# Kernel tuning notes

Hardware: AMD Instinct MI355X
Metric: run time of the kernel (lower is better)

Reference implementation:

```python
import jax, jax.numpy as jnp
import numpy as np

B, P, LANE_LEN = 16, 512, 20
C, T, H, DEPTH = 128, 64, 192, 3
NTL, NLT = 9, 20


def _mlp(x, w1, b1, w2, b2):
    h = jax.nn.gelu(x @ w1 + b1, approximate=False)  # torch nn.GELU = exact erf
    return h @ w2 + b2


def _ln(x, w, b, eps=1e-5):
    m = x.mean(-1, keepdims=True)
    v = jnp.var(x, axis=-1, keepdims=True)
    return (x - m) * jax.lax.rsqrt(v + eps) * w + b


def setup_inputs() -> dict:
    key = jax.random.key(0)
    ks = iter(jax.random.split(key, 40))

    def p(*shape):
        return 0.02 * jax.random.normal(next(ks), shape, dtype=jnp.float32)

    return {
        'x': jax.random.normal(next(ks), (B, P, LANE_LEN, 5), dtype=jnp.float32),
        'tl_table': p(NTL, C),
        'lane_table': p(NLT, C),
        'ch_fc1_w': p(4, C), 'ch_fc1_b': jnp.zeros(C),
        'ch_fc2_w': p(C, C), 'ch_fc2_b': jnp.zeros(C),
        'tok_fc1_w': p(LANE_LEN, T), 'tok_fc1_b': jnp.zeros(T),
        'tok_fc2_w': p(T, T), 'tok_fc2_b': jnp.zeros(T),
        'blk_norm1_w': jnp.ones((DEPTH, C)), 'blk_norm1_b': jnp.zeros((DEPTH, C)),
        'blk_tok_fc1_w': p(DEPTH, T, T), 'blk_tok_fc1_b': jnp.zeros((DEPTH, T)),
        'blk_tok_fc2_w': p(DEPTH, T, T), 'blk_tok_fc2_b': jnp.zeros((DEPTH, T)),
        'blk_norm2_w': jnp.ones((DEPTH, C)), 'blk_norm2_b': jnp.zeros((DEPTH, C)),
        'blk_ch_fc1_w': p(DEPTH, C, C), 'blk_ch_fc1_b': jnp.zeros((DEPTH, C)),
        'blk_ch_fc2_w': p(DEPTH, C, C), 'blk_ch_fc2_b': jnp.zeros((DEPTH, C)),
        'norm_w': jnp.ones(C), 'norm_b': jnp.zeros(C),
        'emb_fc1_w': p(C, H), 'emb_fc1_b': jnp.zeros(H),
        'emb_fc2_w': p(H, H), 'emb_fc2_b': jnp.zeros(H),
    }


def reference(x, tl_table, lane_table, ch_fc1_w, ch_fc1_b, ch_fc2_w, ch_fc2_b,
              tok_fc1_w, tok_fc1_b, tok_fc2_w, tok_fc2_b,
              blk_norm1_w, blk_norm1_b, blk_tok_fc1_w, blk_tok_fc1_b,
              blk_tok_fc2_w, blk_tok_fc2_b, blk_norm2_w, blk_norm2_b,
              blk_ch_fc1_w, blk_ch_fc1_b, blk_ch_fc2_w, blk_ch_fc2_b,
              norm_w, norm_b, emb_fc1_w, emb_fc1_b, emb_fc2_w, emb_fc2_b):
    b, p_, v, _ = x.shape
    mid = x[:, :, LANE_LEN // 2, :]  # [B,P,5]
    pos = jnp.stack([mid[..., 0], mid[..., 1], mid[..., 2],
                     mid[..., 3] / (NTL - 1), mid[..., 4] / (NLT - 1)], axis=-1)
    hdg = x[..., 2]
    geom = jnp.concatenate([x[..., 0:2], jnp.cos(hdg)[..., None], jnp.sin(hdg)[..., None]], axis=-1)  # [B,P,V,4]
    mask_v = jnp.sum(geom != 0, axis=-1) == 0
    mask_p = jnp.all(mask_v, axis=-1)  # [B,P] True = fully padded polyline
    valid = (~mask_p).reshape(-1)
    # jit-friendly equivalent of gather->compute->scatter: compute all rows, zero invalid ones
    g = geom.reshape(b * p_, v, 4)
    tl = jnp.clip(x[..., 3].reshape(b * p_, v).astype(jnp.int32), 0, NTL - 1)
    lt = jnp.clip(x[..., 4].reshape(b * p_, v).astype(jnp.int32), 0, NLT - 1)
    f = _mlp(g, ch_fc1_w, ch_fc1_b, ch_fc2_w, ch_fc2_b) + tl_table[tl] + lane_table[lt]  # [N,V,C]
    f = _mlp(f.transpose(0, 2, 1), tok_fc1_w, tok_fc1_b, tok_fc2_w, tok_fc2_b).transpose(0, 2, 1)  # [N,T,C]
    for i in range(DEPTH):
        y = _ln(f, blk_norm1_w[i], blk_norm1_b[i])
        y = _mlp(y.transpose(0, 2, 1), blk_tok_fc1_w[i], blk_tok_fc1_b[i],
                 blk_tok_fc2_w[i], blk_tok_fc2_b[i]).transpose(0, 2, 1)
        f = f + y
        y = _ln(f, blk_norm2_w[i], blk_norm2_b[i])
        f = f + _mlp(y, blk_ch_fc1_w[i], blk_ch_fc1_b[i], blk_ch_fc2_w[i], blk_ch_fc2_b[i])
    f = f.mean(axis=1)  # [N,C]
    f = _mlp(_ln(f, norm_w, norm_b), emb_fc1_w, emb_fc1_b, emb_fc2_w, emb_fc2_b)  # [N,H]
    out = (f * valid[:, None].astype(f.dtype)).reshape(b, p_, H)
    return out, mask_p, pos
```

## Files before the change

kernel.cpp:

```cpp
#include <hip/hip_runtime.h>

#define NROWS 8192
#define V 20
#define C 128
#define T 64
#define HDIM 192
#define DEPTH 3

typedef __attribute__((ext_vector_type(8))) short bf16x8;
typedef __attribute__((ext_vector_type(4))) float floatx4;

#define WS_TOKFC1 0
#define WS_TOKFC2 2048
#define WS_BTOK1  6144
#define WS_BTOK2  18432
#define WS_CHFC2  30720
#define WS_BCH1   47104
#define WS_BCH2   96256
#define WS_TOTAL  145408

__device__ __forceinline__ float bf2f(unsigned short u) {
    union { unsigned int i; float f; } c; c.i = ((unsigned int)u) << 16; return c.f;
}
__device__ __forceinline__ unsigned short f2bf(float f) {
    union { float f; unsigned int i; } c; c.f = f;
    unsigned int r = c.i + 0x7fffu + ((c.i >> 16) & 1u);
    return (unsigned short)(r >> 16);
}
__device__ __forceinline__ float gelu(float x) {
    float u = x * x;
    float p = fmaf(u, 0.044715f, 1.0f);
    float arg = x * p * -2.3022042f;
    float e = __builtin_amdgcn_exp2f(arg);
    return x * __builtin_amdgcn_rcpf(1.0f + e);
}
__device__ __forceinline__ floatx4 mfma16(bf16x8 a, bf16x8 b, floatx4 c) {
    return __builtin_amdgcn_mfma_f32_16x16x32_bf16(a, b, c, 0, 0, 0);
}


__device__ __forceinline__ void ln_reg(const floatx4 (&R)[8],
                                       const float* __restrict__ w,
                                       const float* __restrict__ b,
                                       unsigned short* __restrict__ s1,
                                       int wid, int lrow, int rrow, bool transposed)
{
    float s[4], q[4];
#pragma unroll
    for (int rr = 0; rr < 4; ++rr) {
        float ss = 0.f, qq = 0.f;
#pragma unroll
        for (int nt = 0; nt < 8; ++nt) { float v = R[nt][rr]; ss += v; qq += v * v; }
        s[rr] = ss; q[rr] = qq;
    }
#pragma unroll
    for (int rr = 0; rr < 4; ++rr) {
        s[rr] += __shfl_xor(s[rr], 1);  q[rr] += __shfl_xor(q[rr], 1);
        s[rr] += __shfl_xor(s[rr], 2);  q[rr] += __shfl_xor(q[rr], 2);
        s[rr] += __shfl_xor(s[rr], 4);  q[rr] += __shfl_xor(q[rr], 4);
        s[rr] += __shfl_xor(s[rr], 8);  q[rr] += __shfl_xor(q[rr], 8);
    }
    float m[4], rs[4];
#pragma unroll
    for (int rr = 0; rr < 4; ++rr) {
        m[rr] = s[rr] * (1.f / 128.f);
        rs[rr] = rsqrtf(q[rr] * (1.f / 128.f) - m[rr] * m[rr] + 1e-5f);
    }
#pragma unroll
    for (int nt = 0; nt < 8; ++nt) {
        const int c = 16 * nt + lrow;
        const float wv = w[c], bv = b[c];
#pragma unroll
        for (int rr = 0; rr < 4; ++rr) {
            const int t = 16 * wid + rrow + rr;
            unsigned short o = f2bf((R[nt][rr] - m[rr]) * rs[rr] * wv + bv);
            if (transposed) s1[c * 72 + t] = o;
            else            s1[t * 136 + c] = o;
        }
    }
}

__device__ __forceinline__ void tok_fc1_gelu(unsigned short* __restrict__ s1,
                                             const unsigned short* __restrict__ wB,
                                             const float* __restrict__ bias,
                                             int wid, int lrow, int kq, int rrow)
{
#pragma unroll
    for (int mt = 0; mt < 2; ++mt) {
        bf16x8 at[2];
#pragma unroll
        for (int kc = 0; kc < 2; ++kc)
            at[kc] = *(const bf16x8*)(s1 + (32 * wid + mt * 16 + lrow) * 72 + kc * 32 + kq);
        floatx4 acc[4];
#pragma unroll
        for (int nt = 0; nt < 4; ++nt) acc[nt] = {0.f, 0.f, 0.f, 0.f};
#pragma unroll
        for (int nt = 0; nt < 4; ++nt)
#pragma unroll
            for (int kc = 0; kc < 2; ++kc) {
                bf16x8 b = *(const bf16x8*)(wB + (nt * 16 + lrow) * 64 + kc * 32 + kq);
                acc[nt] = mfma16(at[kc], b, acc[nt]);
            }
#pragma unroll
        for (int nt = 0; nt < 4; ++nt) {
            const int t = nt * 16 + lrow;
            const float bb = bias[t];
#pragma unroll
            for (int rr = 0; rr < 4; ++rr)
                s1[(32 * wid + mt * 16 + rrow + rr) * 72 + t] = f2bf(gelu(acc[nt][rr] + bb));
        }
    }
}

__device__ __forceinline__ void tok_fc2_to_R(const unsigned short* __restrict__ s1,
                                             const unsigned short* __restrict__ wB,
                                             const float* __restrict__ bias,
                                             floatx4 (&R)[8],
                                             int wid, int lrow, int kq, int rrow)
{
    bf16x8 aw[2];
#pragma unroll
    for (int kc = 0; kc < 2; ++kc)
        aw[kc] = *(const bf16x8*)(wB + (16 * wid + lrow) * 64 + kc * 32 + kq);
    float bb[4];
#pragma unroll
    for (int rr = 0; rr < 4; ++rr) bb[rr] = bias[16 * wid + rrow + rr];
#pragma unroll
    for (int nt = 0; nt < 8; ++nt) {
        floatx4 acc = R[nt];
#pragma unroll
        for (int kc = 0; kc < 2; ++kc) {
            bf16x8 b = *(const bf16x8*)(s1 + (16 * nt + lrow) * 72 + kc * 32 + kq);
            acc = mfma16(aw[kc], b, acc);
        }
#pragma unroll
        for (int rr = 0; rr < 4; ++rr) acc[rr] += bb[rr];
        R[nt] = acc;
    }
}

__device__ __forceinline__ void ch_fc1_gelu(unsigned short* __restrict__ s1,
                                            const unsigned short* __restrict__ wB,
                                            const float* __restrict__ bias,
                                            int wid, int lrow, int kq, int rrow)
{
    bf16x8 a2[4];
    const int m = 16 * wid + lrow;
#pragma unroll
    for (int kc = 0; kc < 4; ++kc)
        a2[kc] = *(const bf16x8*)(s1 + m * 136 + kc * 32 + kq);
#pragma unroll
    for (int g = 0; g < 4; ++g) {
        floatx4 acc[2];
#pragma unroll
        for (int i = 0; i < 2; ++i) acc[i] = {0.f, 0.f, 0.f, 0.f};
#pragma unroll
        for (int i = 0; i < 2; ++i) {
            const int n = (2 * g + i) * 16 + lrow;
#pragma unroll
            for (int kc = 0; kc < 4; ++kc) {
                bf16x8 b = *(const bf16x8*)(wB + n * 128 + kc * 32 + kq);
                acc[i] = mfma16(a2[kc], b, acc[i]);
            }
        }
#pragma unroll
        for (int i = 0; i < 2; ++i) {
            const int c = (2 * g + i) * 16 + lrow;
            const float bb = bias[c];
#pragma unroll
            for (int rr = 0; rr < 4; ++rr)
                s1[(16 * wid + rrow + rr) * 136 + c] = f2bf(gelu(acc[i][rr] + bb));
        }
    }
}

__device__ __forceinline__ void ch_fc2_to_R(const unsigned short* __restrict__ s1,
                                            const unsigned short* __restrict__ wB,
                                            const float* __restrict__ bias,
                                            floatx4 (&R)[8],
                                            int wid, int lrow, int kq, int rrow)
{
    bf16x8 a2[4];
    const int m = 16 * wid + lrow;
#pragma unroll
    for (int kc = 0; kc < 4; ++kc)
        a2[kc] = *(const bf16x8*)(s1 + m * 136 + kc * 32 + kq);
#pragma unroll
    for (int nt = 0; nt < 8; ++nt) {
        floatx4 acc = R[nt];
        const float bb = bias[16 * nt + lrow];
#pragma unroll
        for (int kc = 0; kc < 4; ++kc) {
            bf16x8 b = *(const bf16x8*)(wB + (16 * nt + lrow) * 128 + kc * 32 + kq);
            acc = mfma16(a2[kc], b, acc);
        }
#pragma unroll
        for (int rr = 0; rr < 4; ++rr) acc[rr] += bb;
        R[nt] = acc;
    }
}

__device__ __forceinline__ void layer_norm_to(const float* __restrict__ sF,
                                              unsigned short* __restrict__ sA,
                                              const float* __restrict__ w,
                                              const float* __restrict__ b,
                                              int tid, bool transposed, int strideOut)
{
    const int t = tid >> 2, part = tid & 3;
    const float* row = sF + t * 132 + part * 32;
    float s = 0.f, q = 0.f;
#pragma unroll
    for (int j = 0; j < 8; ++j) {
        float4 v = *(const float4*)(row + j * 4);
        s += (v.x + v.y) + (v.z + v.w);
        q += v.x * v.x + v.y * v.y + v.z * v.z + v.w * v.w;
    }
    s += __shfl_xor(s, 1); q += __shfl_xor(q, 1);
    s += __shfl_xor(s, 2); q += __shfl_xor(q, 2);
    const float m = s * (1.f / 128.f);
    const float rs = rsqrtf(q * (1.f / 128.f) - m * m + 1e-5f);
#pragma unroll
    for (int j = 0; j < 8; ++j) {
        float4 v = *(const float4*)(row + j * 4);
        const int c = part * 32 + j * 4;
        float4 wv = *(const float4*)(w + c);
        float4 bv = *(const float4*)(b + c);
        unsigned short o0 = f2bf((v.x - m) * rs * wv.x + bv.x);
        unsigned short o1 = f2bf((v.y - m) * rs * wv.y + bv.y);
        unsigned short o2 = f2bf((v.z - m) * rs * wv.z + bv.z);
        unsigned short o3 = f2bf((v.w - m) * rs * wv.w + bv.w);
        if (transposed) {
            sA[(c + 0) * strideOut + t] = o0;
            sA[(c + 1) * strideOut + t] = o1;
            sA[(c + 2) * strideOut + t] = o2;
            sA[(c + 3) * strideOut + t] = o3;
        } else {
            ushort4 pk; pk.x = o0; pk.y = o1; pk.z = o2; pk.w = o3;
            *(ushort4*)(sA + t * strideOut + c) = pk;
        }
    }
}

__global__ void prep_weights(const float* __restrict__ tokfc1,
                             const float* __restrict__ tokfc2,
                             const float* __restrict__ btok1,
                             const float* __restrict__ btok2,
                             const float* __restrict__ chfc2,
                             const float* __restrict__ bch1,
                             const float* __restrict__ bch2,
                             unsigned short* __restrict__ ws)
{
    int idx = blockIdx.x * 256 + threadIdx.x;
    if (idx >= WS_TOTAL) return;
    if (idx < 2048) {
        int n = idx >> 5, k = idx & 31;
        ws[WS_TOKFC1 + idx] = (k < V) ? f2bf(tokfc1[k * 64 + n]) : 0;
        return;
    }
    idx -= 2048;
    if (idx < 4096) {
        int n = idx >> 6, k = idx & 63;
        ws[WS_TOKFC2 + idx] = f2bf(tokfc2[k * 64 + n]);
        return;
    }
    idx -= 4096;
    if (idx < 12288) {
        int d = idx >> 12, rem = idx & 4095, n = rem >> 6, k = rem & 63;
        ws[WS_BTOK1 + idx] = f2bf(btok1[d * 4096 + k * 64 + n]);
        return;
    }
    idx -= 12288;
    if (idx < 12288) {
        int d = idx >> 12, rem = idx & 4095, n = rem >> 6, k = rem & 63;
        ws[WS_BTOK2 + idx] = f2bf(btok2[d * 4096 + k * 64 + n]);
        return;
    }
    idx -= 12288;
    if (idx < 16384) {
        int n = idx >> 7, k = idx & 127;
        ws[WS_CHFC2 + idx] = f2bf(chfc2[k * 128 + n]);
        return;
    }
    idx -= 16384;
    if (idx < 49152) {
        int d = idx >> 14, rem = idx & 16383, n = rem >> 7, k = rem & 127;
        ws[WS_BCH1 + idx] = f2bf(bch1[d * 16384 + k * 128 + n]);
        return;
    }
    idx -= 49152;
    {
        int d = idx >> 14, rem = idx & 16383, n = rem >> 7, k = rem & 127;
        ws[WS_BCH2 + idx] = f2bf(bch2[d * 16384 + k * 128 + n]);
    }
}

__global__ __launch_bounds__(256) __attribute__((amdgpu_waves_per_eu(3)))
void lanefusion_mfma(
    const float* __restrict__ x,
    const float* __restrict__ tl_table, const float* __restrict__ lane_table,
    const float* __restrict__ ch_fc1_w, const float* __restrict__ ch_fc1_b,
    const float* __restrict__ ch_fc2_b,
    const float* __restrict__ tok_fc1_b, const float* __restrict__ tok_fc2_b,
    const float* __restrict__ bn1w, const float* __restrict__ bn1b,
    const float* __restrict__ btok1b, const float* __restrict__ btok2b,
    const float* __restrict__ bn2w, const float* __restrict__ bn2b,
    const float* __restrict__ bch1b, const float* __restrict__ bch2b,
    const float* __restrict__ norm_w, const float* __restrict__ norm_b,
    const float* __restrict__ emb1w, const float* __restrict__ emb1b,
    const float* __restrict__ emb2w, const float* __restrict__ emb2b,
    const unsigned short* __restrict__ ws,
    float* __restrict__ out)
{
    __shared__ unsigned short s1[128 * 72];
    __shared__ float sVec[320];
    __shared__ int sTL[V], sLT[V], sMaskV[V];
    __shared__ float sValidF;

    const int tid = threadIdx.x;
    const int r = blockIdx.x;
    const int lane = tid & 63, wid = tid >> 6;
    const int lrow = lane & 15;
    const int kq = (lane >> 4) * 8;
    const int rrow = (lane >> 4) * 4;

    float* outp  = out;
    float* maskp = out + (size_t)NROWS * HDIM;
    float* posp  = maskp + NROWS;

    float* sX = sVec;
    float* sG = sVec + 128;

    {
        uint4* p = (uint4*)s1;
        uint4 z; z.x = z.y = z.z = z.w = 0u;
        for (int i = tid; i < 1152; i += 256) p[i] = z;
    }

    const float* xr = x + (size_t)r * (V * 5);
    if (tid < V * 5) sX[tid] = xr[tid];
    __syncthreads();

    if (tid < V) {
        float x0 = sX[tid * 5 + 0], x1 = sX[tid * 5 + 1], hd = sX[tid * 5 + 2];
        float chv = cosf(hd), shv = sinf(hd);
        sG[tid * 4 + 0] = x0; sG[tid * 4 + 1] = x1;
        sG[tid * 4 + 2] = chv; sG[tid * 4 + 3] = shv;
        int nz = (x0 != 0.f) + (x1 != 0.f) + (chv != 0.f) + (shv != 0.f);
        sMaskV[tid] = (nz == 0);
        int tl = (int)sX[tid * 5 + 3]; tl = tl < 0 ? 0 : (tl > 8 ? 8 : tl);
        int lt = (int)sX[tid * 5 + 4]; lt = lt < 0 ? 0 : (lt > 19 ? 19 : lt);
        sTL[tid] = tl; sLT[tid] = lt;
    }
    __syncthreads();

    if (tid == 0) {
        int mp = 1;
        for (int v = 0; v < V; ++v) mp &= sMaskV[v];
        sValidF = mp ? 0.f : 1.f;
        maskp[r] = mp ? 1.f : 0.f;
        posp[(size_t)r * 5 + 0] = sX[50];
        posp[(size_t)r * 5 + 1] = sX[51];
        posp[(size_t)r * 5 + 2] = sX[52];
        posp[(size_t)r * 5 + 3] = sX[53] * (1.f / 8.f);
        posp[(size_t)r * 5 + 4] = sX[54] * (1.f / 19.f);
    }

    {
        float g0[4], g1[4];
        const bool v1ok = (lrow < 4);
        const int v0 = lrow, v1 = 16 + lrow;
#pragma unroll
        for (int i = 0; i < 4; ++i) {
            g0[i] = sG[v0 * 4 + i];
            g1[i] = v1ok ? sG[v1 * 4 + i] : 0.f;
        }
        floatx4 acc[2][2];
#pragma unroll
        for (int mt = 0; mt < 2; ++mt)
#pragma unroll
            for (int ni = 0; ni < 2; ++ni) acc[mt][ni] = {0.f, 0.f, 0.f, 0.f};
        const unsigned short* wB = ws + WS_CHFC2;
#pragma unroll 1
        for (int kc = 0; kc < 4; ++kc) {
            union { unsigned short u[8]; bf16x8 v; } p0, p1;
            const int kb = kc * 32 + kq;
#pragma unroll
            for (int j = 0; j < 8; ++j) {
                const float w0 = ch_fc1_w[0 * C + kb + j];
                const float w1 = ch_fc1_w[1 * C + kb + j];
                const float w2 = ch_fc1_w[2 * C + kb + j];
                const float w3 = ch_fc1_w[3 * C + kb + j];
                const float bb = ch_fc1_b[kb + j];
                float h0 = fmaf(g0[0], w0, fmaf(g0[1], w1, fmaf(g0[2], w2, fmaf(g0[3], w3, bb))));
                p0.u[j] = f2bf(gelu(h0));
                if (v1ok) {
                    float h1 = fmaf(g1[0], w0, fmaf(g1[1], w1, fmaf(g1[2], w2, fmaf(g1[3], w3, bb))));
                    p1.u[j] = f2bf(gelu(h1));
                } else p1.u[j] = 0;
            }
#pragma unroll
            for (int ni = 0; ni < 2; ++ni) {
                const int n = (2 * wid + ni) * 16 + lrow;
                bf16x8 b = *(const bf16x8*)(wB + n * 128 + kc * 32 + kq);
                acc[0][ni] = mfma16(p0.v, b, acc[0][ni]);
                acc[1][ni] = mfma16(p1.v, b, acc[1][ni]);
            }
        }
#pragma unroll
        for (int ni = 0; ni < 2; ++ni) {
            const int c = (2 * wid + ni) * 16 + lrow;
            const float bb = ch_fc2_b[c];
#pragma unroll
            for (int mt = 0; mt < 2; ++mt)
#pragma unroll
                for (int rr = 0; rr < 4; ++rr) {
                    const int v = mt * 16 + rrow + rr;
                    if (v < V) {
                        float val = acc[mt][ni][rr] + bb
                                  + tl_table[sTL[v] * C + c] + lane_table[sLT[v] * C + c];
                        s1[c * 72 + v] = f2bf(val);
                    }
                }
        }
    }

    {
        bf16x8 af[2];
#pragma unroll
        for (int mt = 0; mt < 2; ++mt) {
            const int m = 32 * wid + mt * 16 + lrow;
            af[mt] = *(const bf16x8*)(s1 + m * 72 + kq);
        }
        floatx4 acc[2][4];
#pragma unroll
        for (int mt = 0; mt < 2; ++mt)
#pragma unroll
            for (int nt = 0; nt < 4; ++nt) acc[mt][nt] = {0.f, 0.f, 0.f, 0.f};
        const unsigned short* wB = ws + WS_TOKFC1;
#pragma unroll
        for (int nt = 0; nt < 4; ++nt) {
            const int n = nt * 16 + lrow;
            bf16x8 b = *(const bf16x8*)(wB + n * 32 + kq);
            acc[0][nt] = mfma16(af[0], b, acc[0][nt]);
            acc[1][nt] = mfma16(af[1], b, acc[1][nt]);
        }
#pragma unroll
        for (int nt = 0; nt < 4; ++nt) {
            const int t = nt * 16 + lrow;
            const float bb = tok_fc1_b[t];
#pragma unroll
            for (int mt = 0; mt < 2; ++mt)
#pragma unroll
                for (int rr = 0; rr < 4; ++rr) {
                    const int m = 32 * wid + mt * 16 + rrow + rr;
                    s1[m * 72 + t] = f2bf(gelu(acc[mt][nt][rr] + bb));
                }
        }
    }
    __syncthreads();

    floatx4 R[8];
#pragma unroll
    for (int nt = 0; nt < 8; ++nt) R[nt] = {0.f, 0.f, 0.f, 0.f};

    tok_fc2_to_R(s1, ws + WS_TOKFC2, tok_fc2_b, R, wid, lrow, kq, rrow);

#pragma unroll 1
    for (int blk = 0; blk < DEPTH; ++blk) {
        __syncthreads();
        ln_reg(R, bn1w + blk * C, bn1b + blk * C, s1, wid, lrow, rrow, true);
        __syncthreads();
        tok_fc1_gelu(s1, ws + WS_BTOK1 + blk * 4096, btok1b + blk * T, wid, lrow, kq, rrow);
        __syncthreads();
        tok_fc2_to_R(s1, ws + WS_BTOK2 + blk * 4096, btok2b + blk * T, R, wid, lrow, kq, rrow);
        __syncthreads();
        ln_reg(R, bn2w + blk * C, bn2b + blk * C, s1, wid, lrow, rrow, false);
        ch_fc1_gelu(s1, ws + WS_BCH1 + blk * 16384, bch1b + blk * C, wid, lrow, kq, rrow);
        ch_fc2_to_R(s1, ws + WS_BCH2 + blk * 16384, bch2b + blk * C, R, wid, lrow, kq, rrow);
    }
    __syncthreads();

    {
        float* P = (float*)s1;
        float snt[8];
#pragma unroll
        for (int nt = 0; nt < 8; ++nt)
            snt[nt] = (R[nt][0] + R[nt][1]) + (R[nt][2] + R[nt][3]);
#pragma unroll
        for (int nt = 0; nt < 8; ++nt) {
            snt[nt] += __shfl_xor(snt[nt], 16);
            snt[nt] += __shfl_xor(snt[nt], 32);
        }
        if (lane < 16) {
#pragma unroll
            for (int nt = 0; nt < 8; ++nt)
                P[wid * 128 + 16 * nt + lane] = snt[nt];
        }
    }
    __syncthreads();
    float fm = 0.f;
    {
        const float* P = (const float*)s1;
        if (tid < C) {
            fm = (P[tid] + P[128 + tid] + P[256 + tid] + P[384 + tid]) * (1.f / 64.f);
            sVec[tid] = fm;
        }
    }
    __syncthreads();
    {
        float s = 0.f, q = 0.f;
#pragma unroll
        for (int c = 0; c < C; c += 4) {
            float4 v = *(const float4*)(sVec + c);
            s += (v.x + v.y) + (v.z + v.w);
            q += v.x * v.x + v.y * v.y + v.z * v.z + v.w * v.w;
        }
        __syncthreads();
        const float m = s * (1.f / 128.f);
        const float rs = rsqrtf(q * (1.f / 128.f) - m * m + 1e-5f);
        if (tid < C) sVec[tid] = (fm - m) * rs * norm_w[tid] + norm_b[tid];
    }
    __syncthreads();

    if (tid < HDIM) {
        float a0 = 0.f, a1 = 0.f, a2 = 0.f, a3 = 0.f;
#pragma unroll 4
        for (int c = 0; c < C; c += 4) {
            float4 sv = *(const float4*)(sVec + c);
            a0 = fmaf(sv.x, emb1w[(c + 0) * HDIM + tid], a0);
            a1 = fmaf(sv.y, emb1w[(c + 1) * HDIM + tid], a1);
            a2 = fmaf(sv.z, emb1w[(c + 2) * HDIM + tid], a2);
            a3 = fmaf(sv.w, emb1w[(c + 3) * HDIM + tid], a3);
        }
        sVec[C + tid] = gelu(((a0 + a1) + (a2 + a3)) + emb1b[tid]);
    }
    __syncthreads();
    if (tid < HDIM) {
        float a0 = 0.f, a1 = 0.f, a2 = 0.f, a3 = 0.f;
#pragma unroll 4
        for (int j = 0; j < HDIM; j += 4) {
            float4 sv = *(const float4*)(sVec + C + j);
            a0 = fmaf(sv.x, emb2w[(j + 0) * HDIM + tid], a0);
            a1 = fmaf(sv.y, emb2w[(j + 1) * HDIM + tid], a1);
            a2 = fmaf(sv.z, emb2w[(j + 2) * HDIM + tid], a2);
            a3 = fmaf(sv.w, emb2w[(j + 3) * HDIM + tid], a3);
        }
        outp[(size_t)r * HDIM + tid] = (((a0 + a1) + (a2 + a3)) + emb2b[tid]) * sValidF;
    }
}

template<int K, int LDA, int N>
__device__ __forceinline__ void gemm_bf(const unsigned short* __restrict__ A,
                                        const float* __restrict__ W,
                                        float acc[4][8])
{
#pragma unroll 2
    for (int k = 0; k < K; k += 4) {
        float a[4][4];
#pragma unroll
        for (int i = 0; i < 4; ++i) {
            ushort4 raw = *(const ushort4*)(A + i * LDA + k);
            a[i][0] = bf2f(raw.x); a[i][1] = bf2f(raw.y);
            a[i][2] = bf2f(raw.z); a[i][3] = bf2f(raw.w);
        }
#pragma unroll
        for (int kk = 0; kk < 4; ++kk) {
            const float* wr = W + (k + kk) * N;
            float4 w0 = *(const float4*)(wr);
            float4 w1 = *(const float4*)(wr + 4);
#pragma unroll
            for (int i = 0; i < 4; ++i) {
                acc[i][0] = fmaf(a[i][kk], w0.x, acc[i][0]);
                acc[i][1] = fmaf(a[i][kk], w0.y, acc[i][1]);
                acc[i][2] = fmaf(a[i][kk], w0.z, acc[i][2]);
                acc[i][3] = fmaf(a[i][kk], w0.w, acc[i][3]);
                acc[i][4] = fmaf(a[i][kk], w1.x, acc[i][4]);
                acc[i][5] = fmaf(a[i][kk], w1.y, acc[i][5]);
                acc[i][6] = fmaf(a[i][kk], w1.z, acc[i][6]);
                acc[i][7] = fmaf(a[i][kk], w1.w, acc[i][7]);
            }
        }
    }
}

template<int K, int LDA, int N>
__device__ __forceinline__ void gemm_f32(const float* __restrict__ A,
                                         const float* __restrict__ W,
                                         float acc[4][8])
{
#pragma unroll
    for (int k = 0; k < K; k += 4) {
        float a[4][4];
#pragma unroll
        for (int i = 0; i < 4; ++i) {
            float4 v = *(const float4*)(A + i * LDA + k);
            a[i][0] = v.x; a[i][1] = v.y; a[i][2] = v.z; a[i][3] = v.w;
        }
#pragma unroll
        for (int kk = 0; kk < 4; ++kk) {
            const float* wr = W + (k + kk) * N;
            float4 w0 = *(const float4*)(wr);
            float4 w1 = *(const float4*)(wr + 4);
#pragma unroll
            for (int i = 0; i < 4; ++i) {
                acc[i][0] = fmaf(a[i][kk], w0.x, acc[i][0]);
                acc[i][1] = fmaf(a[i][kk], w0.y, acc[i][1]);
                acc[i][2] = fmaf(a[i][kk], w0.z, acc[i][2]);
                acc[i][3] = fmaf(a[i][kk], w0.w, acc[i][3]);
                acc[i][4] = fmaf(a[i][kk], w1.x, acc[i][4]);
                acc[i][5] = fmaf(a[i][kk], w1.y, acc[i][5]);
                acc[i][6] = fmaf(a[i][kk], w1.z, acc[i][6]);
                acc[i][7] = fmaf(a[i][kk], w1.w, acc[i][7]);
            }
        }
    }
}

__global__ __launch_bounds__(256, 3)
void lanefusion_scalar(
    const float* __restrict__ x,
    const float* __restrict__ tl_table, const float* __restrict__ lane_table,
    const float* __restrict__ ch_fc1_w, const float* __restrict__ ch_fc1_b,
    const float* __restrict__ ch_fc2_w, const float* __restrict__ ch_fc2_b,
    const float* __restrict__ tok_fc1_w, const float* __restrict__ tok_fc1_b,
    const float* __restrict__ tok_fc2_w, const float* __restrict__ tok_fc2_b,
    const float* __restrict__ bn1w, const float* __restrict__ bn1b,
    const float* __restrict__ btok1w, const float* __restrict__ btok1b,
    const float* __restrict__ btok2w, const float* __restrict__ btok2b,
    const float* __restrict__ bn2w, const float* __restrict__ bn2b,
    const float* __restrict__ bch1w, const float* __restrict__ bch1b,
// ... 153 lines not shown
#pragma unroll
                for (int j = 0; j < 8; ++j)
                    sF[(c0 + j) * 132 + (r0 + i)] += acc[i][j] + btok2b[blk * T + c0 + j];
        }
        __syncthreads();

        layer_norm_to(sF, sA, bn2w + blk * C, bn2b + blk * C, tid, false, 132);
        __syncthreads();
        {
            const int r0 = (tid >> 4) * 4, c0 = (tid & 15) * 8;
            float acc[4][8] = {};
            gemm_bf<128, 132, 128>(sA + r0 * 132, bch1w + blk * C * C + c0, acc);
#pragma unroll
            for (int i = 0; i < 4; ++i)
#pragma unroll
                for (int j = 0; j < 8; ++j)
                    acc[i][j] = gelu(acc[i][j] + bch1b[blk * C + c0 + j]);
            __syncthreads();
#pragma unroll
            for (int i = 0; i < 4; ++i)
#pragma unroll
                for (int j = 0; j < 8; ++j)
                    sA[(r0 + i) * 132 + c0 + j] = f2bf(acc[i][j]);
        }
        __syncthreads();
        {
            const int r0 = (tid >> 4) * 4, c0 = (tid & 15) * 8;
            float acc[4][8] = {};
            gemm_bf<128, 132, 128>(sA + r0 * 132, bch2w + blk * C * C + c0, acc);
#pragma unroll
            for (int i = 0; i < 4; ++i)
#pragma unroll
                for (int j = 0; j < 8; ++j)
                    sF[(r0 + i) * 132 + c0 + j] += acc[i][j] + bch2b[blk * C + c0 + j];
        }
        __syncthreads();
    }

    float fm = 0.f;
    if (tid < C) {
#pragma unroll 8
        for (int t = 0; t < T; ++t) fm += sF[t * 132 + tid];
        fm *= (1.f / 64.f);
        sVec[tid] = fm;
    }
    __syncthreads();
    {
        float s = 0.f, q = 0.f;
        for (int c = 0; c < C; ++c) { float v = sVec[c]; s += v; q += v * v; }
        __syncthreads();
        const float m = s * (1.f / 128.f);
        const float rs = rsqrtf(q * (1.f / 128.f) - m * m + 1e-5f);
        if (tid < C) sVec[tid] = (fm - m) * rs * norm_w[tid] + norm_b[tid];
    }
    __syncthreads();

    if (tid < HDIM) {
        float v1 = emb1b[tid];
        for (int c = 0; c < C; ++c) v1 = fmaf(sVec[c], emb1w[c * HDIM + tid], v1);
        sVec[C + tid] = gelu(v1);
    }
    __syncthreads();
    if (tid < HDIM) {
        float v2 = emb2b[tid];
        for (int j = 0; j < HDIM; ++j) v2 = fmaf(sVec[C + j], emb2w[j * HDIM + tid], v2);
        outp[(size_t)r * HDIM + tid] = v2 * sValidF;
    }
}

extern "C" void kernel_launch(void* const* d_in, const int* in_sizes, int n_in,
                              void* d_out, int out_size, void* d_ws, size_t ws_size,
                              hipStream_t stream) {
    (void)in_sizes; (void)n_in; (void)out_size;
    if (ws_size >= (size_t)WS_TOTAL * 2) {
        prep_weights<<<dim3((WS_TOTAL + 255) / 256), dim3(256), 0, stream>>>(
            (const float*)d_in[7],
            (const float*)d_in[9],
            (const float*)d_in[13],
            (const float*)d_in[15],
            (const float*)d_in[5],
            (const float*)d_in[19],
            (const float*)d_in[21],
            (unsigned short*)d_ws);
        lanefusion_mfma<<<dim3(NROWS), dim3(256), 0, stream>>>(
            (const float*)d_in[0],  (const float*)d_in[1],  (const float*)d_in[2],
            (const float*)d_in[3],  (const float*)d_in[4],
            (const float*)d_in[6],
            (const float*)d_in[8],  (const float*)d_in[10],
            (const float*)d_in[11], (const float*)d_in[12],
            (const float*)d_in[14], (const float*)d_in[16],
            (const float*)d_in[17], (const float*)d_in[18],
            (const float*)d_in[20], (const float*)d_in[22],
            (const float*)d_in[23], (const float*)d_in[24],
            (const float*)d_in[25], (const float*)d_in[26],
            (const float*)d_in[27], (const float*)d_in[28],
            (const unsigned short*)d_ws,
            (float*)d_out);
    } else {
        lanefusion_scalar<<<dim3(NROWS), dim3(256), 0, stream>>>(
            (const float*)d_in[0],  (const float*)d_in[1],  (const float*)d_in[2],
            (const float*)d_in[3],  (const float*)d_in[4],  (const float*)d_in[5],
            (const float*)d_in[6],  (const float*)d_in[7],  (const float*)d_in[8],
            (const float*)d_in[9],  (const float*)d_in[10], (const float*)d_in[11],
            (const float*)d_in[12], (const float*)d_in[13], (const float*)d_in[14],
            (const float*)d_in[15], (const float*)d_in[16], (const float*)d_in[17],
            (const float*)d_in[18], (const float*)d_in[19], (const float*)d_in[20],
            (const float*)d_in[21], (const float*)d_in[22], (const float*)d_in[23],
            (const float*)d_in[24], (const float*)d_in[25], (const float*)d_in[26],
            (const float*)d_in[27], (const float*)d_in[28],
            (float*)d_out);
    }
}
```

Before: 1.192 ms.

## Process two polylines per block with two waves per row and register-reused weight fragments

Each block now handles two rows, with waves split into pairs per row, so each wave computes a 32-row M tile (two MFMA m-tiles). Weight fragments are loaded once and reused across both m-tiles, which halves weight traffic from global/L2 per row, and the grid is halved. In exchange, register pressure rises (R doubles to 16 floatx4), shared memory doubles, and the final embedding MLP is serialized over the two rows.

```diff
diff --git a/kernel.cpp b/kernel.cpp
--- a/kernel.cpp
+++ b/kernel.cpp
@@ -39,164 +39,192 @@
 }
 
 
-__device__ __forceinline__ void ln_reg(const floatx4 (&R)[8],
-                                       const float* __restrict__ w,
-                                       const float* __restrict__ b,
-                                       unsigned short* __restrict__ s1,
-                                       int wid, int lrow, int rrow, bool transposed)
-{
-    float s[4], q[4];
-#pragma unroll
-    for (int rr = 0; rr < 4; ++rr) {
-        float ss = 0.f, qq = 0.f;
-#pragma unroll
-        for (int nt = 0; nt < 8; ++nt) { float v = R[nt][rr]; ss += v; qq += v * v; }
-        s[rr] = ss; q[rr] = qq;
-    }
-#pragma unroll
-    for (int rr = 0; rr < 4; ++rr) {
-        s[rr] += __shfl_xor(s[rr], 1);  q[rr] += __shfl_xor(q[rr], 1);
-        s[rr] += __shfl_xor(s[rr], 2);  q[rr] += __shfl_xor(q[rr], 2);
-        s[rr] += __shfl_xor(s[rr], 4);  q[rr] += __shfl_xor(q[rr], 4);
-        s[rr] += __shfl_xor(s[rr], 8);  q[rr] += __shfl_xor(q[rr], 8);
-    }
-    float m[4], rs[4];
-#pragma unroll
-    for (int rr = 0; rr < 4; ++rr) {
-        m[rr] = s[rr] * (1.f / 128.f);
-        rs[rr] = rsqrtf(q[rr] * (1.f / 128.f) - m[rr] * m[rr] + 1e-5f);
-    }
-#pragma unroll
-    for (int nt = 0; nt < 8; ++nt) {
-        const int c = 16 * nt + lrow;
-        const float wv = w[c], bv = b[c];
+__device__ __forceinline__ void ln_reg2(const floatx4 (&R)[2][8],
+                                        const float* __restrict__ w,
+                                        const float* __restrict__ b,
+                                        unsigned short* __restrict__ s1r,
+                                        int vw, int lrow, int rrow, bool transposed)
+{
+#pragma unroll
+    for (int mt = 0; mt < 2; ++mt) {
+        float s[4], q[4];
 #pragma unroll
         for (int rr = 0; rr < 4; ++rr) {
-            const int t = 16 * wid + rrow + rr;
-            unsigned short o = f2bf((R[nt][rr] - m[rr]) * rs[rr] * wv + bv);
-            if (transposed) s1[c * 72 + t] = o;
-            else            s1[t * 136 + c] = o;
-        }
-    }
-}
-
-__device__ __forceinline__ void tok_fc1_gelu(unsigned short* __restrict__ s1,
-                                             const unsigned short* __restrict__ wB,
-                                             const float* __restrict__ bias,
-                                             int wid, int lrow, int kq, int rrow)
-{
-#pragma unroll
-    for (int mt = 0; mt < 2; ++mt) {
-        bf16x8 at[2];
+            float ss = 0.f, qq = 0.f;
+#pragma unroll
+            for (int nt = 0; nt < 8; ++nt) { float v = R[mt][nt][rr]; ss += v; qq += v * v; }
+            s[rr] = ss; q[rr] = qq;
+        }
+#pragma unroll
+        for (int rr = 0; rr < 4; ++rr) {
+            s[rr] += __shfl_xor(s[rr], 1);  q[rr] += __shfl_xor(q[rr], 1);
+            s[rr] += __shfl_xor(s[rr], 2);  q[rr] += __shfl_xor(q[rr], 2);
+            s[rr] += __shfl_xor(s[rr], 4);  q[rr] += __shfl_xor(q[rr], 4);
+            s[rr] += __shfl_xor(s[rr], 8);  q[rr] += __shfl_xor(q[rr], 8);
+        }
+        float m[4], rs[4];
+#pragma unroll
+        for (int rr = 0; rr < 4; ++rr) {
+            m[rr] = s[rr] * (1.f / 128.f);
+            rs[rr] = rsqrtf(q[rr] * (1.f / 128.f) - m[rr] * m[rr] + 1e-5f);
+        }
+#pragma unroll
+        for (int nt = 0; nt < 8; ++nt) {
+            const int c = 16 * nt + lrow;
+            const float wv = w[c], bv = b[c];
+#pragma unroll
+            for (int rr = 0; rr < 4; ++rr) {
+                const int t = 32 * vw + 16 * mt + rrow + rr;
+                unsigned short o = f2bf((R[mt][nt][rr] - m[rr]) * rs[rr] * wv + bv);
+                if (transposed) s1r[c * 72 + t] = o;
+                else            s1r[t * 136 + c] = o;
+            }
+        }
+    }
+}
+
+__device__ __forceinline__ void tok_fc1_g2(unsigned short* __restrict__ s1r,
+                                           const unsigned short* __restrict__ wB,
+                                           const float* __restrict__ bias,
+                                           int vw, int lrow, int kq, int rrow)
+{
+    bf16x8 bw[4][2];
+#pragma unroll
+    for (int nt = 0; nt < 4; ++nt)
 #pragma unroll
         for (int kc = 0; kc < 2; ++kc)
-            at[kc] = *(const bf16x8*)(s1 + (32 * wid + mt * 16 + lrow) * 72 + kc * 32 + kq);
+            bw[nt][kc] = *(const bf16x8*)(wB + (nt * 16 + lrow) * 64 + kc * 32 + kq);
+#pragma unroll 1
+    for (int mt = 0; mt < 4; ++mt) {
+        const int m = 64 * vw + 16 * mt + lrow;
+        bf16x8 af0 = *(const bf16x8*)(s1r + m * 72 + kq);
+        bf16x8 af1 = *(const bf16x8*)(s1r + m * 72 + 32 + kq);
         floatx4 acc[4];
 #pragma unroll
         for (int nt = 0; nt < 4; ++nt) acc[nt] = {0.f, 0.f, 0.f, 0.f};
 #pragma unroll
-        for (int nt = 0; nt < 4; ++nt)
-#pragma unroll
-            for (int kc = 0; kc < 2; ++kc) {
-                bf16x8 b = *(const bf16x8*)(wB + (nt * 16 + lrow) * 64 + kc * 32 + kq);
-                acc[nt] = mfma16(at[kc], b, acc[nt]);
-            }
+        for (int nt = 0; nt < 4; ++nt) {
+            acc[nt] = mfma16(af0, bw[nt][0], acc[nt]);
+            acc[nt] = mfma16(af1, bw[nt][1], acc[nt]);
+        }
 #pragma unroll
         for (int nt = 0; nt < 4; ++nt) {
             const int t = nt * 16 + lrow;
             const float bb = bias[t];
 #pragma unroll
             for (int rr = 0; rr < 4; ++rr)
-                s1[(32 * wid + mt * 16 + rrow + rr) * 72 + t] = f2bf(gelu(acc[nt][rr] + bb));
-        }
-    }
-}
-
-__device__ __forceinline__ void tok_fc2_to_R(const unsigned short* __restrict__ s1,
-                                             const unsigned short* __restrict__ wB,
-                                             const float* __restrict__ bias,
-                                             floatx4 (&R)[8],
-                                             int wid, int lrow, int kq, int rrow)
-{
-    bf16x8 aw[2];
-#pragma unroll
-    for (int kc = 0; kc < 2; ++kc)
-        aw[kc] = *(const bf16x8*)(wB + (16 * wid + lrow) * 64 + kc * 32 + kq);
-    float bb[4];
-#pragma unroll
-    for (int rr = 0; rr < 4; ++rr) bb[rr] = bias[16 * wid + rrow + rr];
+                s1r[(64 * vw + 16 * mt + rrow + rr) * 72 + t] = f2bf(gelu(acc[nt][rr] + bb));
+        }
+    }
+}
+
+__device__ __forceinline__ void tok_fc2_R2(const unsigned short* __restrict__ s1r,
+                                           const unsigned short* __restrict__ wB,
+                                           const float* __restrict__ bias,
+                                           floatx4 (&R)[2][8],
+                                           int vw, int lrow, int kq, int rrow)
+{
+    bf16x8 aw[2][2];
+#pragma unroll
+    for (int mt = 0; mt < 2; ++mt)
+#pragma unroll
+        for (int kc = 0; kc < 2; ++kc)
+            aw[mt][kc] = *(const bf16x8*)(wB + (32 * vw + 16 * mt + lrow) * 64 + kc * 32 + kq);
+    float bb[2][4];
+#pragma unroll
+    for (int mt = 0; mt < 2; ++mt)
+#pragma unroll
+        for (int rr = 0; rr < 4; ++rr) bb[mt][rr] = bias[32 * vw + 16 * mt + rrow + rr];
 #pragma unroll
     for (int nt = 0; nt < 8; ++nt) {
-        floatx4 acc = R[nt];
-#pragma unroll
-        for (int kc = 0; kc < 2; ++kc) {
-            bf16x8 b = *(const bf16x8*)(s1 + (16 * nt + lrow) * 72 + kc * 32 + kq);
-            acc = mfma16(aw[kc], b, acc);
-        }
-#pragma unroll
-        for (int rr = 0; rr < 4; ++rr) acc[rr] += bb[rr];
-        R[nt] = acc;
-    }
-}
-
-__device__ __forceinline__ void ch_fc1_gelu(unsigned short* __restrict__ s1,
-                                            const unsigned short* __restrict__ wB,
-                                            const float* __restrict__ bias,
-                                            int wid, int lrow, int kq, int rrow)
-{
-    bf16x8 a2[4];
-    const int m = 16 * wid + lrow;
-#pragma unroll
-    for (int kc = 0; kc < 4; ++kc)
-        a2[kc] = *(const bf16x8*)(s1 + m * 136 + kc * 32 + kq);
-#pragma unroll
+        bf16x8 b0 = *(const bf16x8*)(s1r + (16 * nt + lrow) * 72 + kq);
+        bf16x8 b1 = *(const bf16x8*)(s1r + (16 * nt + lrow) * 72 + 32 + kq);
+#pragma unroll
+        for (int mt = 0; mt < 2; ++mt) {
+            floatx4 acc = R[mt][nt];
+            acc = mfma16(aw[mt][0], b0, acc);
+            acc = mfma16(aw[mt][1], b1, acc);
+#pragma unroll
+            for (int rr = 0; rr < 4; ++rr) acc[rr] += bb[mt][rr];
+            R[mt][nt] = acc;
+        }
+    }
+}
+
+__device__ __forceinline__ void ch_fc1_g2(unsigned short* __restrict__ s1r,
+                                          const unsigned short* __restrict__ wB,
+                                          const float* __restrict__ bias,
+                                          int vw, int lrow, int kq, int rrow)
+{
+    bf16x8 a2[2][4];
+#pragma unroll
+    for (int mt = 0; mt < 2; ++mt) {
+        const int m = 32 * vw + 16 * mt + lrow;
+#pragma unroll
+        for (int kc = 0; kc < 4; ++kc)
+            a2[mt][kc] = *(const bf16x8*)(s1r + m * 136 + kc * 32 + kq);
+    }
+#pragma unroll 1
     for (int g = 0; g < 4; ++g) {
-        floatx4 acc[2];
-#pragma unroll
-        for (int i = 0; i < 2; ++i) acc[i] = {0.f, 0.f, 0.f, 0.f};
-#pragma unroll
-        for (int i = 0; i < 2; ++i) {
-            const int n = (2 * g + i) * 16 + lrow;
-#pragma unroll
-            for (int kc = 0; kc < 4; ++kc) {
-                bf16x8 b = *(const bf16x8*)(wB + n * 128 + kc * 32 + kq);
-                acc[i] = mfma16(a2[kc], b, acc[i]);
-            }
-        }
-#pragma unroll
-        for (int i = 0; i < 2; ++i) {
-            const int c = (2 * g + i) * 16 + lrow;
-            const float bb = bias[c];
-#pragma unroll
-            for (int rr = 0; rr < 4; ++rr)
-                s1[(16 * wid + rrow + rr) * 136 + c] = f2bf(gelu(acc[i][rr] + bb));
-        }
-    }
-}
-
-__device__ __forceinline__ void ch_fc2_to_R(const unsigned short* __restrict__ s1,
-                                            const unsigned short* __restrict__ wB,
-                                            const float* __restrict__ bias,
-                                            floatx4 (&R)[8],
-                                            int wid, int lrow, int kq, int rrow)
-{
-    bf16x8 a2[4];
-    const int m = 16 * wid + lrow;
-#pragma unroll
-    for (int kc = 0; kc < 4; ++kc)
-        a2[kc] = *(const bf16x8*)(s1 + m * 136 + kc * 32 + kq);
-#pragma unroll
+        bf16x8 bw[2][4];
+#pragma unroll
+        for (int i = 0; i < 2; ++i)
+#pragma unroll
+            for (int kc = 0; kc < 4; ++kc)
+                bw[i][kc] = *(const bf16x8*)(wB + ((2 * g + i) * 16 + lrow) * 128 + kc * 32 + kq);
+#pragma unroll
+        for (int mt = 0; mt < 2; ++mt) {
+            floatx4 acc[2];
+#pragma unroll
+            for (int i = 0; i < 2; ++i) acc[i] = {0.f, 0.f, 0.f, 0.f};
+#pragma unroll
+            for (int i = 0; i < 2; ++i)
+#pragma unroll
+                for (int kc = 0; kc < 4; ++kc)
+                    acc[i] = mfma16(a2[mt][kc], bw[i][kc], acc[i]);
+#pragma unroll
+            for (int i = 0; i < 2; ++i) {
+                const int c = (2 * g + i) * 16 + lrow;
+                const float bb = bias[c];
+#pragma unroll
+                for (int rr = 0; rr < 4; ++rr)
+                    s1r[(32 * vw + 16 * mt + rrow + rr) * 136 + c] = f2bf(gelu(acc[i][rr] + bb));
+            }
+        }
+    }
+}
+
+__device__ __forceinline__ void ch_fc2_R2(const unsigned short* __restrict__ s1r,
+                                          const unsigned short* __restrict__ wB,
+                                          const float* __restrict__ bias,
+                                          floatx4 (&R)[2][8],
+                                          int vw, int lrow, int kq, int rrow)
+{
+    bf16x8 a2[2][4];
+#pragma unroll
+    for (int mt = 0; mt < 2; ++mt) {
+        const int m = 32 * vw + 16 * mt + lrow;
+#pragma unroll
+        for (int kc = 0; kc < 4; ++kc)
+            a2[mt][kc] = *(const bf16x8*)(s1r + m * 136 + kc * 32 + kq);
+    }
+#pragma unroll 1
     for (int nt = 0; nt < 8; ++nt) {
-        floatx4 acc = R[nt];
+        bf16x8 bw[4];
+#pragma unroll
+        for (int kc = 0; kc < 4; ++kc)
+            bw[kc] = *(const bf16x8*)(wB + (16 * nt + lrow) * 128 + kc * 32 + kq);
         const float bb = bias[16 * nt + lrow];
 #pragma unroll
-        for (int kc = 0; kc < 4; ++kc) {
-            bf16x8 b = *(const bf16x8*)(wB + (16 * nt + lrow) * 128 + kc * 32 + kq);
-            acc = mfma16(a2[kc], b, acc);
-        }
-#pragma unroll
-        for (int rr = 0; rr < 4; ++rr) acc[rr] += bb;
-        R[nt] = acc;
+        for (int mt = 0; mt < 2; ++mt) {
+            floatx4 acc = R[mt][nt];
+#pragma unroll
+            for (int kc = 0; kc < 4; ++kc)
+                acc = mfma16(a2[mt][kc], bw[kc], acc);
+#pragma unroll
+            for (int rr = 0; rr < 4; ++rr) acc[rr] += bb;
+            R[mt][nt] = acc;
+        }
     }
 }
 
@@ -311,61 +339,71 @@
     const unsigned short* __restrict__ ws,
     float* __restrict__ out)
 {
-    __shared__ unsigned short s1[128 * 72];
+    __shared__ unsigned short s1[2 * 9216];
     __shared__ float sVec[320];
-    __shared__ int sTL[V], sLT[V], sMaskV[V];
-    __shared__ float sValidF;
+    __shared__ float sX2[2][100];
+    __shared__ float sG2[2][80];
+    __shared__ int sTL2[2][V], sLT2[2][V], sMaskV2[2][V];
+    __shared__ float sValidF2[2];
 
     const int tid = threadIdx.x;
-    const int r = blockIdx.x;
     const int lane = tid & 63, wid = tid >> 6;
+    const int rsel = wid >> 1;
+    const int vw = wid & 1;
     const int lrow = lane & 15;
     const int kq = (lane >> 4) * 8;
     const int rrow = (lane >> 4) * 4;
+    const size_t r0 = (size_t)blockIdx.x * 2;
 
     float* outp  = out;
     float* maskp = out + (size_t)NROWS * HDIM;
     float* posp  = maskp + NROWS;
 
-    float* sX = sVec;
-    float* sG = sVec + 128;
+    unsigned short* s1r = s1 + rsel * 9216;
 
     {
         uint4* p = (uint4*)s1;
         uint4 z; z.x = z.y = z.z = z.w = 0u;
-        for (int i = tid; i < 1152; i += 256) p[i] = z;
-    }
-
-    const float* xr = x + (size_t)r * (V * 5);
-    if (tid < V * 5) sX[tid] = xr[tid];
-    __syncthreads();
-
-    if (tid < V) {
-        float x0 = sX[tid * 5 + 0], x1 = sX[tid * 5 + 1], hd = sX[tid * 5 + 2];
-        float chv = cosf(hd), shv = sinf(hd);
-        sG[tid * 4 + 0] = x0; sG[tid * 4 + 1] = x1;
-        sG[tid * 4 + 2] = chv; sG[tid * 4 + 3] = shv;
-        int nz = (x0 != 0.f) + (x1 != 0.f) + (chv != 0.f) + (shv != 0.f);
-        sMaskV[tid] = (nz == 0);
-        int tl = (int)sX[tid * 5 + 3]; tl = tl < 0 ? 0 : (tl > 8 ? 8 : tl);
-        int lt = (int)sX[tid * 5 + 4]; lt = lt < 0 ? 0 : (lt > 19 ? 19 : lt);
-        sTL[tid] = tl; sLT[tid] = lt;
-    }
-    __syncthreads();
-
-    if (tid == 0) {
+        for (int i = tid; i < 2304; i += 256) p[i] = z;
+    }
+
+    if (tid < 100)                     sX2[0][tid]       = x[r0 * 100 + tid];
+    else if (tid >= 128 && tid < 228)  sX2[1][tid - 128] = x[(r0 + 1) * 100 + (tid - 128)];
+    __syncthreads();
+
+    {
+        int rowi = -1, v = 0;
+        if (tid < V)                      { rowi = 0; v = tid; }
+        else if (tid >= 128 && tid < 128 + V) { rowi = 1; v = tid - 128; }
+        if (rowi >= 0) {
+            float x0 = sX2[rowi][v * 5 + 0], x1 = sX2[rowi][v * 5 + 1], hd = sX2[rowi][v * 5 + 2];
+            float chv = cosf(hd), shv = sinf(hd);
+            sG2[rowi][v * 4 + 0] = x0; sG2[rowi][v * 4 + 1] = x1;
+            sG2[rowi][v * 4 + 2] = chv; sG2[rowi][v * 4 + 3] = shv;
+            int nz = (x0 != 0.f) + (x1 != 0.f) + (chv != 0.f) + (shv != 0.f);
+            sMaskV2[rowi][v] = (nz == 0);
+            int tl = (int)sX2[rowi][v * 5 + 3]; tl = tl < 0 ? 0 : (tl > 8 ? 8 : tl);
+            int lt = (int)sX2[rowi][v * 5 + 4]; lt = lt < 0 ? 0 : (lt > 19 ? 19 : lt);
+            sTL2[rowi][v] = tl; sLT2[rowi][v] = lt;
+        }
+    }
+    __syncthreads();
+
+    if (tid < 2) {
+        const int rowi = tid;
         int mp = 1;
-        for (int v = 0; v < V; ++v) mp &= sMaskV[v];
-        sValidF = mp ? 0.f : 1.f;
-        maskp[r] = mp ? 1.f : 0.f;
-        posp[(size_t)r * 5 + 0] = sX[50];
-        posp[(size_t)r * 5 + 1] = sX[51];
-        posp[(size_t)r * 5 + 2] = sX[52];
-        posp[(size_t)r * 5 + 3] = sX[53] * (1.f / 8.f);
-        posp[(size_t)r * 5 + 4] = sX[54] * (1.f / 19.f);
+        for (int v = 0; v < V; ++v) mp &= sMaskV2[rowi][v];
+        sValidF2[rowi] = mp ? 0.f : 1.f;
+        maskp[r0 + rowi] = mp ? 1.f : 0.f;
+        posp[(r0 + rowi) * 5 + 0] = sX2[rowi][50];
+        posp[(r0 + rowi) * 5 + 1] = sX2[rowi][51];
+        posp[(r0 + rowi) * 5 + 2] = sX2[rowi][52];
+        posp[(r0 + rowi) * 5 + 3] = sX2[rowi][53] * (1.f / 8.f);
+        posp[(r0 + rowi) * 5 + 4] = sX2[rowi][54] * (1.f / 19.f);
     }
 
     {
+        const float* sG = sG2[rsel];
         float g0[4], g1[4];
         const bool v1ok = (lrow < 4);
         const int v0 = lrow, v1 = 16 + lrow;
@@ -374,11 +412,11 @@
             g0[i] = sG[v0 * 4 + i];
             g1[i] = v1ok ? sG[v1 * 4 + i] : 0.f;
         }
-        floatx4 acc[2][2];
+        floatx4 acc[2][4];
 #pragma unroll
         for (int mt = 0; mt < 2; ++mt)
 #pragma unroll
-            for (int ni = 0; ni < 2; ++ni) acc[mt][ni] = {0.f, 0.f, 0.f, 0.f};
+            for (int ni = 0; ni < 4; ++ni) acc[mt][ni] = {0.f, 0.f, 0.f, 0.f};
         const unsigned short* wB = ws + WS_CHFC2;
 #pragma unroll 1
         for (int kc = 0; kc < 4; ++kc) {
@@ -399,16 +437,16 @@
                 } else p1.u[j] = 0;
             }
 #pragma unroll
-            for (int ni = 0; ni < 2; ++ni) {
-                const int n = (2 * wid + ni) * 16 + lrow;
+            for (int ni = 0; ni < 4; ++ni) {
+                const int n = (4 * vw + ni) * 16 + lrow;
                 bf16x8 b = *(const bf16x8*)(wB + n * 128 + kc * 32 + kq);
                 acc[0][ni] = mfma16(p0.v, b, acc[0][ni]);
                 acc[1][ni] = mfma16(p1.v, b, acc[1][ni]);
             }
         }
 #pragma unroll
-        for (int ni = 0; ni < 2; ++ni) {
-            const int c = (2 * wid + ni) * 16 + lrow;
+        for (int ni = 0; ni < 4; ++ni) {
+            const int c = (4 * vw + ni) * 16 + lrow;
             const float bb = ch_fc2_b[c];
 #pragma unroll
             for (int mt = 0; mt < 2; ++mt)
@@ -417,75 +455,70 @@
                     const int v = mt * 16 + rrow + rr;
                     if (v < V) {
                         float val = acc[mt][ni][rr] + bb
-                                  + tl_table[sTL[v] * C + c] + lane_table[sLT[v] * C + c];
-                        s1[c * 72 + v] = f2bf(val);
+                                  + tl_table[sTL2[rsel][v] * C + c] + lane_table[sLT2[rsel][v] * C + c];
+                        s1r[c * 72 + v] = f2bf(val);
                     }
                 }
         }
     }
 
     {
-        bf16x8 af[2];
-#pragma unroll
-        for (int mt = 0; mt < 2; ++mt) {
-            const int m = 32 * wid + mt * 16 + lrow;
-            af[mt] = *(const bf16x8*)(s1 + m * 72 + kq);
-        }
-        floatx4 acc[2][4];
-#pragma unroll
-        for (int mt = 0; mt < 2; ++mt)
-#pragma unroll
-            for (int nt = 0; nt < 4; ++nt) acc[mt][nt] = {0.f, 0.f, 0.f, 0.f};
+        bf16x8 bw[4];
         const unsigned short* wB = ws + WS_TOKFC1;
 #pragma unroll
-        for (int nt = 0; nt < 4; ++nt) {
-            const int n = nt * 16 + lrow;
-            bf16x8 b = *(const bf16x8*)(wB + n * 32 + kq);
-            acc[0][nt] = mfma16(af[0], b, acc[0][nt]);
-            acc[1][nt] = mfma16(af[1], b, acc[1][nt]);
-        }
-#pragma unroll
-        for (int nt = 0; nt < 4; ++nt) {
-            const int t = nt * 16 + lrow;
-            const float bb = tok_fc1_b[t];
-#pragma unroll
-            for (int mt = 0; mt < 2; ++mt)
-#pragma unroll
-                for (int rr = 0; rr < 4; ++rr) {
-                    const int m = 32 * wid + mt * 16 + rrow + rr;
-                    s1[m * 72 + t] = f2bf(gelu(acc[mt][nt][rr] + bb));
-                }
-        }
-    }
-    __syncthreads();
-
-    floatx4 R[8];
-#pragma unroll
-    for (int nt = 0; nt < 8; ++nt) R[nt] = {0.f, 0.f, 0.f, 0.f};
-
-    tok_fc2_to_R(s1, ws + WS_TOKFC2, tok_fc2_b, R, wid, lrow, kq, rrow);
+        for (int nt = 0; nt < 4; ++nt)
+            bw[nt] = *(const bf16x8*)(wB + (nt * 16 + lrow) * 32 + kq);
+#pragma unroll 1
+        for (int mt = 0; mt < 4; ++mt) {
+            const int m = 64 * vw + 16 * mt + lrow;
+            bf16x8 af = *(const bf16x8*)(s1r + m * 72 + kq);
+            floatx4 acc[4];
+#pragma unroll
+            for (int nt = 0; nt < 4; ++nt) acc[nt] = {0.f, 0.f, 0.f, 0.f};
+#pragma unroll
+            for (int nt = 0; nt < 4; ++nt) acc[nt] = mfma16(af, bw[nt], acc[nt]);
+#pragma unroll
+            for (int nt = 0; nt < 4; ++nt) {
+                const int t = nt * 16 + lrow;
+                const float bb = tok_fc1_b[t];
+#pragma unroll
+                for (int rr = 0; rr < 4; ++rr)
+                    s1r[(64 * vw + 16 * mt + rrow + rr) * 72 + t] = f2bf(gelu(acc[nt][rr] + bb));
+            }
+        }
+    }
+    __syncthreads();
+
+    floatx4 R[2][8];
+#pragma unroll
+    for (int mt = 0; mt < 2; ++mt)
+#pragma unroll
+        for (int nt = 0; nt < 8; ++nt) R[mt][nt] = {0.f, 0.f, 0.f, 0.f};
+
+    tok_fc2_R2(s1r, ws + WS_TOKFC2, tok_fc2_b, R, vw, lrow, kq, rrow);
 
 #pragma unroll 1
     for (int blk = 0; blk < DEPTH; ++blk) {
         __syncthreads();
-        ln_reg(R, bn1w + blk * C, bn1b + blk * C, s1, wid, lrow, rrow, true);
-        __syncthreads();
-        tok_fc1_gelu(s1, ws + WS_BTOK1 + blk * 4096, btok1b + blk * T, wid, lrow, kq, rrow);
-        __syncthreads();
-        tok_fc2_to_R(s1, ws + WS_BTOK2 + blk * 4096, btok2b + blk * T, R, wid, lrow, kq, rrow);
-        __syncthreads();
-        ln_reg(R, bn2w + blk * C, bn2b + blk * C, s1, wid, lrow, rrow, false);
-        ch_fc1_gelu(s1, ws + WS_BCH1 + blk * 16384, bch1b + blk * C, wid, lrow, kq, rrow);
-        ch_fc2_to_R(s1, ws + WS_BCH2 + blk * 16384, bch2b + blk * C, R, wid, lrow, kq, rrow);
-    }
-    __syncthreads();
-
+        ln_reg2(R, bn1w + blk * C, bn1b + blk * C, s1r, vw, lrow, rrow, true);
+        __syncthreads();
+        tok_fc1_g2(s1r, ws + WS_BTOK1 + blk * 4096, btok1b + blk * T, vw, lrow, kq, rrow);
+        __syncthreads();
+        tok_fc2_R2(s1r, ws + WS_BTOK2 + blk * 4096, btok2b + blk * T, R, vw, lrow, kq, rrow);
+        __syncthreads();
+        ln_reg2(R, bn2w + blk * C, bn2b + blk * C, s1r, vw, lrow, rrow, false);
+        ch_fc1_g2(s1r, ws + WS_BCH1 + blk * 16384, bch1b + blk * C, vw, lrow, kq, rrow);
+        ch_fc2_R2(s1r, ws + WS_BCH2 + blk * 16384, bch2b + blk * C, R, vw, lrow, kq, rrow);
+    }
+    __syncthreads();
+
+    float* P = (float*)s1;
     {
-        float* P = (float*)s1;
         float snt[8];
 #pragma unroll
         for (int nt = 0; nt < 8; ++nt)
-            snt[nt] = (R[nt][0] + R[nt][1]) + (R[nt][2] + R[nt][3]);
+            snt[nt] = ((R[0][nt][0] + R[0][nt][1]) + (R[0][nt][2] + R[0][nt][3]))
+                    + ((R[1][nt][0] + R[1][nt][1]) + (R[1][nt][2] + R[1][nt][3]));
 #pragma unroll
         for (int nt = 0; nt < 8; ++nt) {
             snt[nt] += __shfl_xor(snt[nt], 16);
@@ -494,58 +527,60 @@
         if (lane < 16) {
 #pragma unroll
             for (int nt = 0; nt < 8; ++nt)
-                P[wid * 128 + 16 * nt + lane] = snt[nt];
-        }
-    }
-    __syncthreads();
-    float fm = 0.f;
-    {
-        const float* P = (const float*)s1;
+                P[rsel * 256 + vw * 128 + 16 * nt + lane] = snt[nt];
+        }
+    }
+    __syncthreads();
+
+#pragma unroll 1
+    for (int rowi = 0; rowi < 2; ++rowi) {
+        float fm = 0.f;
         if (tid < C) {
-            fm = (P[tid] + P[128 + tid] + P[256 + tid] + P[384 + tid]) * (1.f / 64.f);
+            fm = (P[rowi * 256 + tid] + P[rowi * 256 + 128 + tid]) * (1.f / 64.f);
             sVec[tid] = fm;
         }
-    }
-    __syncthreads();
-    {
-        float s = 0.f, q = 0.f;
-#pragma unroll
-        for (int c = 0; c < C; c += 4) {
-            float4 v = *(const float4*)(sVec + c);
-            s += (v.x + v.y) + (v.z + v.w);
-            q += v.x * v.x + v.y * v.y + v.z * v.z + v.w * v.w;
-        }
-        __syncthreads();
-        const float m = s * (1.f / 128.f);
-        const float rs = rsqrtf(q * (1.f / 128.f) - m * m + 1e-5f);
-        if (tid < C) sVec[tid] = (fm - m) * rs * norm_w[tid] + norm_b[tid];
-    }
-    __syncthreads();
-
-    if (tid < HDIM) {
-        float a0 = 0.f, a1 = 0.f, a2 = 0.f, a3 = 0.f;
+        __syncthreads();
+        {
+            float s = 0.f, q = 0.f;
+#pragma unroll
+            for (int c = 0; c < C; c += 4) {
+                float4 v = *(const float4*)(sVec + c);
+                s += (v.x + v.y) + (v.z + v.w);
+                q += v.x * v.x + v.y * v.y + v.z * v.z + v.w * v.w;
+            }
+            __syncthreads();
+            const float m = s * (1.f / 128.f);
+            const float rs = rsqrtf(q * (1.f / 128.f) - m * m + 1e-5f);
+            if (tid < C) sVec[tid] = (fm - m) * rs * norm_w[tid] + norm_b[tid];
+        }
+        __syncthreads();
+
+        if (tid < HDIM) {
+            float a0 = 0.f, a1 = 0.f, a2 = 0.f, a3 = 0.f;
 #pragma unroll 4
-        for (int c = 0; c < C; c += 4) {
-            float4 sv = *(const float4*)(sVec + c);
-            a0 = fmaf(sv.x, emb1w[(c + 0) * HDIM + tid], a0);
-            a1 = fmaf(sv.y, emb1w[(c + 1) * HDIM + tid], a1);
-            a2 = fmaf(sv.z, emb1w[(c + 2) * HDIM + tid], a2);
-            a3 = fmaf(sv.w, emb1w[(c + 3) * HDIM + tid], a3);
-        }
-        sVec[C + tid] = gelu(((a0 + a1) + (a2 + a3)) + emb1b[tid]);
-    }
-    __syncthreads();
-    if (tid < HDIM) {
-        float a0 = 0.f, a1 = 0.f, a2 = 0.f, a3 = 0.f;
+            for (int c = 0; c < C; c += 4) {
+                float4 sv = *(const float4*)(sVec + c);
+                a0 = fmaf(sv.x, emb1w[(c + 0) * HDIM + tid], a0);
+                a1 = fmaf(sv.y, emb1w[(c + 1) * HDIM + tid], a1);
+                a2 = fmaf(sv.z, emb1w[(c + 2) * HDIM + tid], a2);
+                a3 = fmaf(sv.w, emb1w[(c + 3) * HDIM + tid], a3);
+            }
+            sVec[C + tid] = gelu(((a0 + a1) + (a2 + a3)) + emb1b[tid]);
+        }
+        __syncthreads();
+        if (tid < HDIM) {
+            float a0 = 0.f, a1 = 0.f, a2 = 0.f, a3 = 0.f;
 #pragma unroll 4
-        for (int j = 0; j < HDIM; j += 4) {
-            float4 sv = *(const float4*)(sVec + C + j);
-            a0 = fmaf(sv.x, emb2w[(j + 0) * HDIM + tid], a0);
-            a1 = fmaf(sv.y, emb2w[(j + 1) * HDIM + tid], a1);
-            a2 = fmaf(sv.z, emb2w[(j + 2) * HDIM + tid], a2);
-            a3 = fmaf(sv.w, emb2w[(j + 3) * HDIM + tid], a3);
-        }
-        outp[(size_t)r * HDIM + tid] = (((a0 + a1) + (a2 + a3)) + emb2b[tid]) * sValidF;
+            for (int j = 0; j < HDIM; j += 4) {
+                float4 sv = *(const float4*)(sVec + C + j);
+                a0 = fmaf(sv.x, emb2w[(j + 0) * HDIM + tid], a0);
+                a1 = fmaf(sv.y, emb2w[(j + 1) * HDIM + tid], a1);
+                a2 = fmaf(sv.z, emb2w[(j + 2) * HDIM + tid], a2);
+                a3 = fmaf(sv.w, emb2w[(j + 3) * HDIM + tid], a3);
+            }
+            outp[(r0 + rowi) * HDIM + tid] = (((a0 + a1) + (a2 + a3)) + emb2b[tid]) * sValidF2[rowi];
+        }
+        __syncthreads();
     }
 }
 
@@ -865,7 +900,7 @@
             (const float*)d_in[19],
             (const float*)d_in[21],
             (unsigned short*)d_ws);
-        lanefusion_mfma<<<dim3(NROWS), dim3(256), 0, stream>>>(
+        lanefusion_mfma<<<dim3(NROWS / 2), dim3(256), 0, stream>>>(
             (const float*)d_in[0],  (const float*)d_in[1],  (const float*)d_in[2],
             (const float*)d_in[3],  (const float*)d_in[4],
             (const float*)d_in[6],
```

New measurement: 1.247 ms. 4.6% more time.
